# Optimization experiments

Measured on AMD Instinct MI355X. Metric: run time of the kernel, lower is better.

Reference implementation:

```python
import jax, jax.numpy as jnp
import numpy as np

N_NODES = 10000
N_EDGES = 160000
T_STEPS = 2
N_SAMPLE = 2
H_DIM = 64
Z_DIM = 32
K_HEADS = 4
N_IN = 4


def setup_inputs() -> dict:
    key = jax.random.key(0)
    ks = jax.random.split(key, 16)
    sc = lambda fan_in: 1.0 / np.sqrt(fan_in).astype(np.float32)
    inp = {}
    inp["inputs"] = jax.random.normal(ks[0], (N_NODES, T_STEPS, N_IN), jnp.float32)
    inp["zA"] = jax.random.normal(ks[1], (N_NODES, N_SAMPLE, Z_DIM), jnp.float32)
    inp["zG"] = jax.random.normal(ks[2], (N_NODES, N_SAMPLE, Z_DIM), jnp.float32)
    inp["src"] = jax.random.randint(ks[3], (N_EDGES,), 0, N_NODES)
    inp["dst"] = jax.random.randint(ks[4], (N_EDGES,), 0, N_NODES)
    # GAT attention projections (K heads, no bias): Linear(z_dim -> h_dim)
    inp["Ws"] = jax.random.normal(ks[5], (K_HEADS, H_DIM, Z_DIM), jnp.float32) * sc(Z_DIM)
    inp["Wd"] = jax.random.normal(ks[6], (K_HEADS, H_DIM, Z_DIM), jnp.float32) * sc(Z_DIM)
    # F2: Linear(2h -> h, no bias), ReLU, Linear(h -> h, no bias)
    inp["F2_w1"] = jax.random.normal(ks[7], (H_DIM, 2 * H_DIM), jnp.float32) * sc(2 * H_DIM)
    inp["F2_w2"] = jax.random.normal(ks[8], (H_DIM, H_DIM), jnp.float32) * sc(H_DIM)
    # F1: Linear(K*h -> h, no bias), ReLU, Linear(h -> h, no bias)
    inp["F1_w1"] = jax.random.normal(ks[9], (H_DIM, K_HEADS * H_DIM), jnp.float32) * sc(K_HEADS * H_DIM)
    inp["F1_w2"] = jax.random.normal(ks[10], (H_DIM, H_DIM), jnp.float32) * sc(H_DIM)
    # x_enc: Linear(n_in -> h) with bias
    inp["xenc_w"] = jax.random.normal(ks[11], (H_DIM, N_IN), jnp.float32) * sc(N_IN)
    inp["xenc_b"] = jnp.zeros((H_DIM,), jnp.float32)
    # out_fc: Linear(h+z -> h), ReLU, Linear(h -> 4)
    inp["out_w1"] = jax.random.normal(ks[12], (H_DIM, H_DIM + Z_DIM), jnp.float32) * sc(H_DIM + Z_DIM)
    inp["out_b1"] = jnp.zeros((H_DIM,), jnp.float32)
    inp["out_w2"] = jax.random.normal(ks[13], (4, H_DIM), jnp.float32) * sc(H_DIM)
    inp["out_b2"] = jnp.zeros((4,), jnp.float32)
    inp["pred_steps"] = 2
    return inp


def reference(inputs, zA, zG, src, dst, Ws, Wd, F2_w1, F2_w2, F1_w1, F1_w2,
              xenc_w, xenc_b, out_w1, out_b1, out_w2, out_b2, pred_steps):
    N, T, _ = inputs.shape
    S = zA.shape[1]
    K = Ws.shape[0]

    # --- edge attention (GAT.attn), computed once per forward ---
    As = jnp.einsum('nsz,khz->nskh', zG, Ws)          # [N, S, K, H]
    Ad = jnp.einsum('nsz,khz->nskh', zG, Wd)
    e = jnp.sum(As[src] * Ad[dst], axis=-1)           # [E, S, K]
    e = jax.nn.leaky_relu(e, 0.01)
    # per-destination softmax over incoming edges (DGL mailbox softmax over dim=1)
    m = jax.ops.segment_max(e, dst, num_segments=N)
    ex = jnp.exp(e - m[dst])
    denom = jax.ops.segment_sum(ex, dst, num_segments=N)
    alpha = ex / denom[dst]                           # [E, S, K]
    deg = jax.ops.segment_sum(jnp.ones((e.shape[0],), e.dtype), dst, num_segments=N)
    deg = jnp.maximum(deg, 1.0)[:, None, None]        # [N, 1, 1]; mean over mailbox dim

    def step(xt):
        xt_enc = xt @ xenc_w.T + xenc_b               # [N, S, H]
        cat = jnp.concatenate([xt_enc[src], xt_enc[dst]], axis=-1)  # [E, S, 2H]
        dA = jax.nn.relu(cat @ F2_w1.T) @ F2_w2.T     # [E, S, H]
        # per-head attention-weighted mean over in-neighbors; loop over K (small, fixed)
        res = [jax.ops.segment_sum(alpha[:, :, k:k + 1] * dA, dst, num_segments=N) / deg
               for k in range(K)]
        res = jnp.concatenate(res, axis=-1)           # [N, S, K*H]
        deltax = jax.nn.relu(res @ F1_w1.T) @ F1_w2.T # [N, S, H]
        h = jnp.concatenate([deltax, zA], axis=-1)    # [N, S, H+Z]
        dx = jax.nn.relu(h @ out_w1.T + out_b1) @ out_w2.T + out_b2  # [N, S, 4]
        return xt + dx

    inp_t = jnp.transpose(inputs, (1, 0, 2))          # [T, N, n_in]
    inp_t = jnp.broadcast_to(inp_t[:, :, None, :], (T, N, S, inp_t.shape[-1]))
    preds = []
    for b in range(0, T, pred_steps):                 # blocks of pred_steps
        xt = inp_t[b]
        for _ in range(pred_steps):
            xt = step(xt)
            preds.append(xt)
    out = jnp.stack(preds, axis=0)                    # [T, N, S, 4]
    return jnp.transpose(out, (1, 0, 2, 3))           # [N, T, S, 4]
```

## Files before the change

### kernel.cpp

```cpp
#include <hip/hip_runtime.h>

#define NN 10000
#define NE 160000
#define TT 2
#define SS 2
#define HH 64
#define ZZ 32
#define KK 4
#define NIN 4

typedef short bf16x8 __attribute__((ext_vector_type(8)));
typedef float f32x4 __attribute__((ext_vector_type(4)));

__device__ __forceinline__ unsigned short f2b(float x) {
    unsigned u = __float_as_uint(x);
    u += 0x7fffu + ((u >> 16) & 1u);
    return (unsigned short)(u >> 16);
}
__device__ __forceinline__ float bf2f(unsigned short u) {
    return __uint_as_float(((unsigned)u) << 16);
}

__device__ __forceinline__ float edge_score(const unsigned* __restrict__ zp,
                                            const float* __restrict__ qf) {
    float a = 0.f;
#pragma unroll
    for (int j = 0; j < 16; ++j) {
        unsigned u = zp[j];
        a += __uint_as_float(u << 16) * qf[2*j]
           + __uint_as_float(u & 0xffff0000u) * qf[2*j+1];
    }
    return a > 0.f ? a : 0.01f*a;
}

__global__ __launch_bounds__(256) void k_prep(
    const float* __restrict__ Ws, const float* __restrict__ Wd,
    const float* __restrict__ F2w1, const float* __restrict__ xw,
    const float* __restrict__ xb, const float* __restrict__ F2w2,
    const float* __restrict__ F1w1, const float* __restrict__ F1w2,
    const float* __restrict__ ow1, const float* __restrict__ ow2,
    const float* __restrict__ zA, const float* __restrict__ zG,
    const float* __restrict__ inputs, const int* __restrict__ dst,
    float* __restrict__ MT, float* __restrict__ G1, float* __restrict__ G2,
    float* __restrict__ c1, float* __restrict__ c2,
    unsigned short* __restrict__ W2b, unsigned short* __restrict__ F1w1b,
    unsigned short* __restrict__ F1w2b, unsigned short* __restrict__ ow1b,
    unsigned short* __restrict__ ow2b, unsigned short* __restrict__ zAb,
    unsigned short* __restrict__ zGb, float* __restrict__ xt,
    int* __restrict__ deg_i)
{
    int b = blockIdx.x;
    int tid = threadIdx.x;
    if (b < 16) {
        int o = b*256 + tid;
        int j = o & 31, i = (o >> 5) & 31, k = o >> 10;
        float acc = 0.0f;
        for (int h = 0; h < HH; ++h)
            acc += Ws[(k*HH + h)*ZZ + i] * Wd[(k*HH + h)*ZZ + j];
        MT[(k*ZZ + j)*ZZ + i] = acc;
    } else if (b == 16) {
        int h = tid >> 2, i = tid & 3;
        float a1 = 0.f, a2 = 0.f;
        for (int j = 0; j < HH; ++j) {
            float x = xw[j*NIN + i];
            a1 += F2w1[h*128 + j] * x;
            a2 += F2w1[h*128 + 64 + j] * x;
        }
        G1[h*4 + i] = a1;
        G2[h*4 + i] = a2;
        if (i == 0) {
            float b1 = 0.f, b2 = 0.f;
            for (int j = 0; j < HH; ++j) {
                float bb = xb[j];
                b1 += F2w1[h*128 + j] * bb;
                b2 += F2w1[h*128 + 64 + j] * bb;
            }
            c1[h] = b1; c2[h] = b2;
        }
    } else {
        int t = (b - 17)*256 + tid;
        if (t < NN*SS*ZZ) { zAb[t] = f2b(zA[t]); zGb[t] = f2b(zG[t]); }
        if (t < HH*HH)    { W2b[t] = f2b(F2w2[t]); F1w2b[t] = f2b(F1w2[t]); }
        if (t < HH*KK*HH) F1w1b[t] = f2b(F1w1[t]);
        if (t < HH*(HH+ZZ)) ow1b[t] = f2b(ow1[t]);
        if (t < 4*HH)     ow2b[t] = f2b(ow2[t]);
        if (t < NN*SS*NIN) {
            int i = t & 3;
            int n = t >> 3;
            xt[t] = inputs[n*(TT*NIN) + i];
        }
        if (t < NE) atomicAdd(deg_i + dst[t], 1);
    }
}

__global__ void k_qd(const float* __restrict__ zG, const float* __restrict__ MT,
                     unsigned short* __restrict__ qdb) {
    int t = blockIdx.x * blockDim.x + threadIdx.x;
    if (t >= NN*SS*KK*ZZ) return;
    int i  = t & 31;
    int k  = (t >> 5) & 3;
    int ns = t >> 7;
    const float* zg = zG + ns*ZZ;
    const float* mt = MT + k*ZZ*ZZ;
    float acc = 0.0f;
#pragma unroll
    for (int j = 0; j < ZZ; ++j) acc += mt[j*ZZ + i] * zg[j];
    qdb[t] = f2b(acc);
}

__global__ void k_scan(const int* __restrict__ deg_i, int* __restrict__ offsets,
                       int* __restrict__ cursor) {
    __shared__ int buf0[1024], buf1[1024];
    int tidx = threadIdx.x;
    const int CH = (NN + 1023) / 1024;
    int b0 = tidx * CH;
    int sum = 0;
    for (int i = 0; i < CH; ++i) { int idx = b0 + i; if (idx < NN) sum += deg_i[idx]; }
    buf0[tidx] = sum;
    __syncthreads();
    int* s = buf0; int* d = buf1;
    for (int off = 1; off < 1024; off <<= 1) {
        d[tidx] = s[tidx] + (tidx >= off ? s[tidx - off] : 0);
        __syncthreads();
        int* tmp = s; s = d; d = tmp;
    }
    int run = s[tidx] - sum;
    for (int i = 0; i < CH; ++i) {
        int idx = b0 + i;
        if (idx < NN) { offsets[idx] = run; cursor[idx] = run; run += deg_i[idx]; }
    }
    if (tidx == 0) offsets[NN] = NE;
}

__global__ void k_scatter(const int* __restrict__ src, const int* __restrict__ dst,
                          int* __restrict__ cursor, int* __restrict__ src_by_pos) {
    int e = blockIdx.x * blockDim.x + threadIdx.x;
    if (e >= NE) return;
    int pos = atomicAdd(cursor + dst[e], 1);
    src_by_pos[pos] = src[e];
}

__global__ __launch_bounds__(64) void k_attn_alpha(
    const unsigned short* __restrict__ qdb, const unsigned short* __restrict__ zGb,
    const int* __restrict__ src_by_pos, const int* __restrict__ offsets,
    float* __restrict__ alpha)
{
    int item = blockIdx.x;
    int n = item >> 1, s = item & 1;
    int l = threadIdx.x;
    int i = l >> 2, k = l & 3;
    int r0 = offsets[n], r1 = offsets[n+1];
    float qf[32];
    const unsigned* qp = (const unsigned*)(qdb + (item*KK + k)*ZZ);
#pragma unroll
    for (int j = 0; j < 16; ++j) {
        unsigned u = qp[j];
        qf[2*j]   = __uint_as_float(u << 16);
        qf[2*j+1] = __uint_as_float(u & 0xffff0000u);
    }
    float E[8];
    float mx = -1e30f;
    int nit = 0;
    for (int idx = r0 + i; idx < r1; idx += 16, ++nit) {
        int sn = src_by_pos[idx];
        float e = edge_score((const unsigned*)(zGb + (sn*SS + s)*ZZ), qf);
        if (nit < 8) E[nit] = e;
        mx = fmaxf(mx, e);
    }
#pragma unroll
    for (int off = 4; off < 64; off <<= 1) mx = fmaxf(mx, __shfl_xor(mx, off));
    float sum = 0.f;
    nit = 0;
    for (int idx = r0 + i; idx < r1; idx += 16, ++nit) {
        float e = (nit < 8) ? E[nit]
                : edge_score((const unsigned*)(zGb + (src_by_pos[idx]*SS + s)*ZZ), qf);
        sum += __expf(e - mx);
    }
#pragma unroll
    for (int off = 4; off < 64; off <<= 1) sum += __shfl_xor(sum, off);
    int deg = r1 - r0;
    float dd = (float)(deg > 1 ? deg : 1);
    float inv = sum > 0.f ? 1.f/(sum*dd) : 0.f;
    nit = 0;
    for (int idx = r0 + i; idx < r1; idx += 16, ++nit) {
        float e = (nit < 8) ? E[nit]
                : edge_score((const unsigned*)(zGb + (src_by_pos[idx]*SS + s)*ZZ), qf);
        alpha[(idx*2 + s)*4 + k] = __expf(e - mx) * inv;
    }
}

__global__ __launch_bounds__(64) void k_agg2(
    const float* __restrict__ xt, const float* __restrict__ G1,
    const float* __restrict__ G2, const float* __restrict__ c1,
    const float* __restrict__ c2, const int* __restrict__ src_by_pos,
    const int* __restrict__ offsets, const float* __restrict__ alpha,
    unsigned short* __restrict__ agg_b)
{
    int item = blockIdx.x;
    int n = item >> 1, s = item & 1;
    int h = threadIdx.x;
    int r0 = offsets[n], r1 = offsets[n+1];
    const float4 g1 = *(const float4*)(G1 + h*4);
    const float4 g2 = *(const float4*)(G2 + h*4);
    const float4 xd = *(const float4*)(xt + item*4);
    float p2 = c2[h] + xd.x*g2.x + xd.y*g2.y + xd.z*g2.z + xd.w*g2.w;
    float c1h = c1[h];
    float a0 = 0.f, a1 = 0.f, a2 = 0.f, a3 = 0.f;
    int idx = r0;
    for (; idx + 4 <= r1; idx += 4) {
        int sn0 = src_by_pos[idx];
        int sn1 = src_by_pos[idx+1];
        int sn2 = src_by_pos[idx+2];
        int sn3 = src_by_pos[idx+3];
        float4 x0 = *(const float4*)(xt + (sn0*SS + s)*NIN);
        float4 x1 = *(const float4*)(xt + (sn1*SS + s)*NIN);
        float4 x2 = *(const float4*)(xt + (sn2*SS + s)*NIN);
        float4 x3 = *(const float4*)(xt + (sn3*SS + s)*NIN);
        float4 w0 = *(const float4*)(alpha + ((idx+0)*2 + s)*4);
        float4 w1 = *(const float4*)(alpha + ((idx+1)*2 + s)*4);
        float4 w2 = *(const float4*)(alpha + ((idx+2)*2 + s)*4);
        float4 w3 = *(const float4*)(alpha + ((idx+3)*2 + s)*4);
        float p, hd;
        p = c1h + x0.x*g1.x + x0.y*g1.y + x0.z*g1.z + x0.w*g1.w;
        hd = p + p2; hd = hd > 0.f ? hd : 0.f;
        a0 += w0.x*hd; a1 += w0.y*hd; a2 += w0.z*hd; a3 += w0.w*hd;
        p = c1h + x1.x*g1.x + x1.y*g1.y + x1.z*g1.z + x1.w*g1.w;
        hd = p + p2; hd = hd > 0.f ? hd : 0.f;
        a0 += w1.x*hd; a1 += w1.y*hd; a2 += w1.z*hd; a3 += w1.w*hd;
        p = c1h + x2.x*g1.x + x2.y*g1.y + x2.z*g1.z + x2.w*g1.w;
        hd = p + p2; hd = hd > 0.f ? hd : 0.f;
        a0 += w2.x*hd; a1 += w2.y*hd; a2 += w2.z*hd; a3 += w2.w*hd;
        p = c1h + x3.x*g1.x + x3.y*g1.y + x3.z*g1.z + x3.w*g1.w;
        hd = p + p2; hd = hd > 0.f ? hd : 0.f;
        a0 += w3.x*hd; a1 += w3.y*hd; a2 += w3.z*hd; a3 += w3.w*hd;
    }
    for (; idx < r1; ++idx) {
        int sn = src_by_pos[idx];
        float4 x0 = *(const float4*)(xt + (sn*SS + s)*NIN);
        float4 w0 = *(const float4*)(alpha + (idx*2 + s)*4);
        float p = c1h + x0.x*g1.x + x0.y*g1.y + x0.z*g1.z + x0.w*g1.w;
        float hd = p + p2; hd = hd > 0.f ? hd : 0.f;
        a0 += w0.x*hd; a1 += w0.y*hd; a2 += w0.z*hd; a3 += w0.w*hd;
    }
    agg_b[item*256 +       h] = f2b(a0);
    agg_b[item*256 + 64  + h] = f2b(a1);
    agg_b[item*256 + 128 + h] = f2b(a2);
    agg_b[item*256 + 192 + h] = f2b(a3);
}

__global__ __launch_bounds__(256) void k_node_mfma(
    const unsigned short* __restrict__ agg_b, const unsigned short* __restrict__ zAb,
    const unsigned short* __restrict__ W2b,
    const unsigned short* __restrict__ F1w1b, const unsigned short* __restrict__ F1w2b,
    const unsigned short* __restrict__ ow1b, const unsigned short* __restrict__ ow2b,
    const float* __restrict__ ob1, const float* __restrict__ ob2,
    float* __restrict__ xt, float* __restrict__ out, int tstep)
{
    __shared__ unsigned short res_s[4][16*264];
    __shared__ unsigned short hid_s[4][16*72];
    __shared__ unsigned short hcat_s[4][16*104];
    int tid = threadIdx.x;
    int w = tid >> 6, l = tid & 63, l15 = l & 15, qq = l >> 4;

    bf16x8 w2f[2][4], b2f[2][4], o1f[3][4], bo2[2];
#pragma unroll
    for (int nb = 0; nb < 4; ++nb) {
        int n = nb*16 + l15;
#pragma unroll
        for (int kb = 0; kb < 2; ++kb) {
            w2f[kb][nb] = *(const bf16x8*)(W2b  + n*64 + kb*32 + qq*8);
            b2f[kb][nb] = *(const bf16x8*)(F1w2b + n*64 + kb*32 + qq*8);
        }
#pragma unroll
        for (int kb = 0; kb < 3; ++kb)
            o1f[kb][nb] = *(const bf16x8*)(ow1b + n*96 + kb*32 + qq*8);
    }
#pragma unroll
    for (int kb = 0; kb < 2; ++kb) {
        if (l15 < 4) bo2[kb] = *(const bf16x8*)(ow2b + l15*64 + kb*32 + qq*8);
        else {
            bf16x8 z;
#pragma unroll
            for (int j = 0; j < 8; ++j) z[j] = 0;
            bo2[kb] = z;
        }
    }
    float b1v[4];
#pragma unroll
    for (int nb = 0; nb < 4; ++nb) b1v[nb] = ob1[nb*16 + l15];
    float b2v = (l15 < 4) ? ob2[l15] : 0.0f;

    int itemBase = blockIdx.x*64 + w*16;
    if (itemBase >= NN*SS) return;

    *(uint4*)(&hcat_s[w][l15*104 + 64 + qq*8]) =
        *(const uint4*)(zAb + (itemBase + l15)*ZZ + qq*8);

#pragma unroll
    for (int k = 0; k < 4; ++k) {
        f32x4 acc0[4];
#pragma unroll
        for (int nb = 0; nb < 4; ++nb) acc0[nb] = (f32x4)(0.0f);
#pragma unroll
        for (int kb = 0; kb < 2; ++kb) {
            bf16x8 af = *(const bf16x8*)(agg_b + (itemBase + l15)*256 + k*64 + kb*32 + qq*8);
#pragma unroll
            for (int nb = 0; nb < 4; ++nb)
                acc0[nb] = __builtin_amdgcn_mfma_f32_16x16x32_bf16(af, w2f[kb][nb], acc0[nb], 0, 0, 0);
        }
#pragma unroll
        for (int nb = 0; nb < 4; ++nb)
#pragma unroll
            for (int r = 0; r < 4; ++r)
                res_s[w][(qq*4 + r)*264 + k*64 + nb*16 + l15] = f2b(acc0[nb][r]);
    }

    f32x4 acc[4];
#pragma unroll
    for (int nb = 0; nb < 4; ++nb) acc[nb] = (f32x4)(0.0f);
#pragma unroll
    for (int kb = 0; kb < 8; ++kb) {
        bf16x8 af = *(const bf16x8*)(&res_s[w][l15*264 + kb*32 + qq*8]);
#pragma unroll
        for (int nb = 0; nb < 4; ++nb) {
            bf16x8 bf = *(const bf16x8*)(F1w1b + (nb*16 + l15)*256 + kb*32 + qq*8);
            acc[nb] = __builtin_amdgcn_mfma_f32_16x16x32_bf16(af, bf, acc[nb], 0, 0, 0);
        }
    }
#pragma unroll
    for (int nb = 0; nb < 4; ++nb)
#pragma unroll
        for (int r = 0; r < 4; ++r) {
            float v = acc[nb][r];
            hid_s[w][(qq*4 + r)*72 + nb*16 + l15] = f2b(v > 0.0f ? v : 0.0f);
        }

    f32x4 acc2[4];
#pragma unroll
    for (int nb = 0; nb < 4; ++nb) acc2[nb] = (f32x4)(0.0f);
#pragma unroll
    for (int kb = 0; kb < 2; ++kb) {
        bf16x8 af = *(const bf16x8*)(&hid_s[w][l15*72 + kb*32 + qq*8]);
#pragma unroll
        for (int nb = 0; nb < 4; ++nb)
            acc2[nb] = __builtin_amdgcn_mfma_f32_16x16x32_bf16(af, b2f[kb][nb], acc2[nb], 0, 0, 0);
    }
#pragma unroll
    for (int nb = 0; nb < 4; ++nb)
#pragma unroll
        for (int r = 0; r < 4; ++r)
            hcat_s[w][(qq*4 + r)*104 + nb*16 + l15] = f2b(acc2[nb][r]);

    f32x4 acc3[4];
#pragma unroll
    for (int nb = 0; nb < 4; ++nb) acc3[nb] = (f32x4)(0.0f);
#pragma unroll
    for (int kb = 0; kb < 3; ++kb) {
        bf16x8 af = *(const bf16x8*)(&hcat_s[w][l15*104 + kb*32 + qq*8]);
#pragma unroll
        for (int nb = 0; nb < 4; ++nb)
            acc3[nb] = __builtin_amdgcn_mfma_f32_16x16x32_bf16(af, o1f[kb][nb], acc3[nb], 0, 0, 0);
    }
#pragma unroll
    for (int nb = 0; nb < 4; ++nb)
#pragma unroll
        for (int r = 0; r < 4; ++r) {
            float v = acc3[nb][r] + b1v[nb];
            hid_s[w][(qq*4 + r)*72 + nb*16 + l15] = f2b(v > 0.0f ? v : 0.0f);
        }

    f32x4 acc4 = (f32x4)(0.0f);
#pragma unroll
    for (int kb = 0; kb < 2; ++kb) {
        bf16x8 af = *(const bf16x8*)(&hid_s[w][l15*72 + kb*32 + qq*8]);
        acc4 = __builtin_amdgcn_mfma_f32_16x16x32_bf16(af, bo2[kb], acc4, 0, 0, 0);
    }
    if (l15 < 4) {
#pragma unroll
        for (int r = 0; r < 4; ++r) {
            int item = itemBase + qq*4 + r;
            float nx = xt[item*4 + l15] + acc4[r] + b2v;
            xt[item*4 + l15] = nx;
            int n = item >> 1, s = item & 1;
            out[((n*TT + tstep)*SS + s)*4 + l15] = nx;
        }
    }
}

extern "C" void kernel_launch(void* const* d_in, const int* in_sizes, int n_in,
                              void* d_out, int out_size, void* d_ws, size_t ws_size,
                              hipStream_t stream) {
    const float* inputs = (const float*)d_in[0];
    const float* zA     = (const float*)d_in[1];
    const float* zG     = (const float*)d_in[2];
    const int*   src    = (const int*)d_in[3];
    const int*   dst    = (const int*)d_in[4];
    const float* Ws     = (const float*)d_in[5];
    const float* Wd     = (const float*)d_in[6];
    const float* F2w1   = (const float*)d_in[7];
    const float* F2w2   = (const float*)d_in[8];
    const float* F1w1   = (const float*)d_in[9];
    const float* F1w2   = (const float*)d_in[10];
    const float* xw     = (const float*)d_in[11];
    const float* xb     = (const float*)d_in[12];
    const float* ow1    = (const float*)d_in[13];
    const float* ob1    = (const float*)d_in[14];
    const float* ow2    = (const float*)d_in[15];
    const float* ob2    = (const float*)d_in[16];
    float* out = (float*)d_out;

    float*          base        = (float*)d_ws;
    float*          MT          = base;
    float*          alpha       = base + 4096;
    int*            deg_i       = (int*)(base + 1284096);
    int*            offsets     = (int*)(base + 1294096);
    int*            cursor      = (int*)(base + 1304112);
    int*            src_by_pos  = (int*)(base + 1314112);
    float*          xt          = base + 1474112;
    float*          G1f         = base + 1554112;
    float*          G2f         = base + 1554368;
    float*          c1f         = base + 1554624;
    float*          c2f         = base + 1554688;
    unsigned short* W2b         = (unsigned short*)(base + 1554816);
    unsigned short* F1w1b       = (unsigned short*)(base + 1556864);
    unsigned short* F1w2b       = (unsigned short*)(base + 1565056);
    unsigned short* ow1b        = (unsigned short*)(base + 1567104);
    unsigned short* ow2b        = (unsigned short*)(base + 1570176);
    unsigned short* zAb         = (unsigned short*)(base + 1570304);
    unsigned short* zGb         = (unsigned short*)(base + 1890304);
    unsigned short* agg_b       = (unsigned short*)(base + 2210304);
    unsigned short* qdb         = (unsigned short*)(base + 4770304);

    hipMemsetAsync(deg_i, 0, 10000u * 4u, stream);

    const int CONVB = (NN*SS*ZZ + 255)/256;
    k_prep<<<17 + CONVB, 256, 0, stream>>>(Ws, Wd, F2w1, xw, xb, F2w2, F1w1, F1w2,
                                           ow1, ow2, zA, zG, inputs, dst,
                                           MT, G1f, G2f, c1f, c2f,
                                           W2b, F1w1b, F1w2b, ow1b, ow2b,
                                           zAb, zGb, xt, deg_i);
    k_qd<<<(NN*SS*KK*ZZ + 255)/256, 256, 0, stream>>>(zG, MT, qdb);
    k_scan<<<1, 1024, 0, stream>>>(deg_i, offsets, cursor);
    k_scatter<<<(NE + 255)/256, 256, 0, stream>>>(src, dst, cursor, src_by_pos);
    k_attn_alpha<<<NN*SS, 64, 0, stream>>>(qdb, zGb, src_by_pos, offsets, alpha);

    for (int t = 0; t < 2; ++t) {
        k_agg2<<<NN*SS, 64, 0, stream>>>(xt, G1f, G2f, c1f, c2f,
                                         src_by_pos, offsets, alpha, agg_b);
        k_node_mfma<<<(NN*SS + 63)/64, 256, 0, stream>>>(agg_b, zAb, W2b, F1w1b, F1w2b,
                                                         ow1b, ow2b, ob1, ob2, xt, out, t);
    }
}
```

Before: 251.1 us.

## Fuse query projection and first-step aggregation into attention kernel

Removes the separate k_qd launch by computing each node-sample's per-head query projection in shared memory inside the attention kernel. That kernel also performs the first timestep's edge aggregation directly, reading the just-computed alpha values from shared memory for the first 64 edges. This drops two kernel launches and one global round trip of qdb and alpha. In exchange, the MT projection is recomputed per block from fp32 instead of a bf16 buffer, and the attention kernel grows heavier.

```diff
diff --git a/kernel.cpp b/kernel.cpp
--- a/kernel.cpp
+++ b/kernel.cpp
@@ -93,21 +93,6 @@
     }
 }
 
-__global__ void k_qd(const float* __restrict__ zG, const float* __restrict__ MT,
-                     unsigned short* __restrict__ qdb) {
-    int t = blockIdx.x * blockDim.x + threadIdx.x;
-    if (t >= NN*SS*KK*ZZ) return;
-    int i  = t & 31;
-    int k  = (t >> 5) & 3;
-    int ns = t >> 7;
-    const float* zg = zG + ns*ZZ;
-    const float* mt = MT + k*ZZ*ZZ;
-    float acc = 0.0f;
-#pragma unroll
-    for (int j = 0; j < ZZ; ++j) acc += mt[j*ZZ + i] * zg[j];
-    qdb[t] = f2b(acc);
-}
-
 __global__ void k_scan(const int* __restrict__ deg_i, int* __restrict__ offsets,
                        int* __restrict__ cursor) {
     __shared__ int buf0[1024], buf1[1024];
@@ -140,24 +125,42 @@
     src_by_pos[pos] = src[e];
 }
 
-__global__ __launch_bounds__(64) void k_attn_alpha(
-    const unsigned short* __restrict__ qdb, const unsigned short* __restrict__ zGb,
-    const int* __restrict__ src_by_pos, const int* __restrict__ offsets,
-    float* __restrict__ alpha)
+__global__ __launch_bounds__(64) void k_attn_agg0(
+    const float* __restrict__ MT, const float* __restrict__ zG,
+    const unsigned short* __restrict__ zGb, const int* __restrict__ src_by_pos,
+    const int* __restrict__ offsets, const float* __restrict__ xt,
+    const float* __restrict__ G1, const float* __restrict__ G2,
+    const float* __restrict__ c1, const float* __restrict__ c2,
+    float* alpha, unsigned short* __restrict__ agg_b)
 {
+    __shared__ float sq[128];
+    __shared__ float alpha_s[64][4];
     int item = blockIdx.x;
     int n = item >> 1, s = item & 1;
     int l = threadIdx.x;
     int i = l >> 2, k = l & 3;
     int r0 = offsets[n], r1 = offsets[n+1];
+
+    {
+        int i0 = l & 31;
+        int k0 = l >> 5;
+        int k1 = k0 + 2;
+        const float* zg = zG + item*ZZ;
+        float acc0 = 0.f, acc1 = 0.f;
+#pragma unroll
+        for (int j = 0; j < ZZ; ++j) {
+            float z = zg[j];
+            acc0 += MT[(k0*ZZ + j)*ZZ + i0] * z;
+            acc1 += MT[(k1*ZZ + j)*ZZ + i0] * z;
+        }
+        sq[k0*ZZ + i0] = acc0;
+        sq[k1*ZZ + i0] = acc1;
+    }
+    __syncthreads();
     float qf[32];
-    const unsigned* qp = (const unsigned*)(qdb + (item*KK + k)*ZZ);
-#pragma unroll
-    for (int j = 0; j < 16; ++j) {
-        unsigned u = qp[j];
-        qf[2*j]   = __uint_as_float(u << 16);
-        qf[2*j+1] = __uint_as_float(u & 0xffff0000u);
-    }
+#pragma unroll
+    for (int j = 0; j < 32; ++j) qf[j] = sq[k*ZZ + j];
+
     float E[8];
     float mx = -1e30f;
     int nit = 0;
@@ -185,8 +188,35 @@
     for (int idx = r0 + i; idx < r1; idx += 16, ++nit) {
         float e = (nit < 8) ? E[nit]
                 : edge_score((const unsigned*)(zGb + (src_by_pos[idx]*SS + s)*ZZ), qf);
-        alpha[(idx*2 + s)*4 + k] = __expf(e - mx) * inv;
-    }
+        float a = __expf(e - mx) * inv;
+        alpha[(idx*2 + s)*4 + k] = a;
+        int jo = idx - r0;
+        if (jo < 64) alpha_s[jo][k] = a;
+    }
+    __threadfence_block();
+    __syncthreads();
+
+    int h = l;
+    const float4 g1 = *(const float4*)(G1 + h*4);
+    const float4 g2 = *(const float4*)(G2 + h*4);
+    const float4 xd = *(const float4*)(xt + item*4);
+    float p2 = c2[h] + xd.x*g2.x + xd.y*g2.y + xd.z*g2.z + xd.w*g2.w;
+    float c1h = c1[h];
+    float a0 = 0.f, a1 = 0.f, a2 = 0.f, a3 = 0.f;
+    for (int jo = 0; jo < deg; ++jo) {
+        int idx = r0 + jo;
+        int sn = src_by_pos[idx];
+        float4 x0 = *(const float4*)(xt + (sn*SS + s)*NIN);
+        float4 w4 = (jo < 64) ? *(const float4*)(&alpha_s[jo][0])
+                              : *(const float4*)(alpha + (idx*2 + s)*4);
+        float p = c1h + x0.x*g1.x + x0.y*g1.y + x0.z*g1.z + x0.w*g1.w;
+        float hd = p + p2; hd = hd > 0.f ? hd : 0.f;
+        a0 += w4.x*hd; a1 += w4.y*hd; a2 += w4.z*hd; a3 += w4.w*hd;
+    }
+    agg_b[item*256 +       h] = f2b(a0);
+    agg_b[item*256 + 64  + h] = f2b(a1);
+    agg_b[item*256 + 128 + h] = f2b(a2);
+    agg_b[item*256 + 192 + h] = f2b(a3);
 }
 
 __global__ __launch_bounds__(64) void k_agg2(
@@ -429,7 +459,6 @@
     unsigned short* zAb         = (unsigned short*)(base + 1570304);
     unsigned short* zGb         = (unsigned short*)(base + 1890304);
     unsigned short* agg_b       = (unsigned short*)(base + 2210304);
-    unsigned short* qdb         = (unsigned short*)(base + 4770304);
 
     hipMemsetAsync(deg_i, 0, 10000u * 4u, stream);
 
@@ -439,15 +468,15 @@
                                            MT, G1f, G2f, c1f, c2f,
                                            W2b, F1w1b, F1w2b, ow1b, ow2b,
                                            zAb, zGb, xt, deg_i);
-    k_qd<<<(NN*SS*KK*ZZ + 255)/256, 256, 0, stream>>>(zG, MT, qdb);
     k_scan<<<1, 1024, 0, stream>>>(deg_i, offsets, cursor);
     k_scatter<<<(NE + 255)/256, 256, 0, stream>>>(src, dst, cursor, src_by_pos);
-    k_attn_alpha<<<NN*SS, 64, 0, stream>>>(qdb, zGb, src_by_pos, offsets, alpha);
-
-    for (int t = 0; t < 2; ++t) {
-        k_agg2<<<NN*SS, 64, 0, stream>>>(xt, G1f, G2f, c1f, c2f,
-                                         src_by_pos, offsets, alpha, agg_b);
-        k_node_mfma<<<(NN*SS + 63)/64, 256, 0, stream>>>(agg_b, zAb, W2b, F1w1b, F1w2b,
-                                                         ow1b, ow2b, ob1, ob2, xt, out, t);
-    }
-}
+
+    k_attn_agg0<<<NN*SS, 64, 0, stream>>>(MT, zG, zGb, src_by_pos, offsets, xt,
+                                          G1f, G2f, c1f, c2f, alpha, agg_b);
+    k_node_mfma<<<(NN*SS + 63)/64, 256, 0, stream>>>(agg_b, zAb, W2b, F1w1b, F1w2b,
+                                                     ow1b, ow2b, ob1, ob2, xt, out, 0);
+    k_agg2<<<NN*SS, 64, 0, stream>>>(xt, G1f, G2f, c1f, c2f,
+                                     src_by_pos, offsets, alpha, agg_b);
+    k_node_mfma<<<(NN*SS + 63)/64, 256, 0, stream>>>(agg_b, zAb, W2b, F1w1b, F1w2b,
+                                                     ow1b, ow2b, ob1, ob2, xt, out, 1);
+}
```

Measured after the change: 226.9 us. -9.6%, faster.
